# Optimization experiments

Hardware: AMD Instinct MI355X
Metric: run time of the kernel (lower is better)

## Reference

```python
import jax, jax.numpy as jnp
import numpy as np

B, D, LEAVES, MID = 131072, 256, 4, 2


def setup_inputs() -> dict:
    key = jax.random.key(0)
    ks = jax.random.split(key, 5)
    s = 1.0 / np.sqrt(D).astype(np.float32)
    return {
        "x": jax.random.normal(ks[0], (B, D), jnp.float32),
        "Wg": jax.random.normal(ks[1], (D, LEAVES), jnp.float32) * s,
        "bg": jnp.zeros((LEAVES,), jnp.float32),
        "W_leaf": jax.random.normal(ks[2], (LEAVES, D, D), jnp.float32) * s,
        "b_leaf": jnp.zeros((LEAVES, D), jnp.float32),
        "W_mid": jax.random.normal(ks[3], (MID, D, D), jnp.float32) * s,
        "b_mid": jnp.zeros((MID, D), jnp.float32),
        "W_root": jax.random.normal(ks[4], (D, D), jnp.float32) * s,
        "b_root": jnp.zeros((D,), jnp.float32),
    }


def reference(x, Wg, bg, W_leaf, b_leaf, W_mid, b_mid, W_root, b_root):
    # Gate: argmax over leaf experts (torch.max(...).indices over dim=1)
    logits = x @ Wg + bg                      # [B, LEAVES]
    idx = jnp.argmax(logits, axis=1)          # [B] leaf expert per sample
    pidx = idx // 2                           # [B] parent (mid-level) node on the path

    # Leaf level: compute all 4 leaf experts (small E), select routed one.
    h1_all = jax.nn.relu(jnp.einsum('bd,edh->beh', x, W_leaf) + b_leaf)   # [B,4,D]
    h1 = jnp.take_along_axis(h1_all, idx[:, None, None], axis=1)[:, 0]    # [B,D]

    # Mid level: the parent of the selected leaf.
    h2_all = jax.nn.relu(jnp.einsum('bd,pdh->bph', h1, W_mid) + b_mid)    # [B,2,D]
    h2 = jnp.take_along_axis(h2_all, pidx[:, None, None], axis=1)[:, 0]   # [B,D]

    # Root (shared by all paths). end is None -> returned directly.
    return jax.nn.relu(h2 @ W_root + b_root)                              # [B,D]
```

## Files before the change

kernel.cpp:

```cpp
#include <hip/hip_runtime.h>
#include <hip/hip_bf16.h>
#include <stdint.h>

#define B_ROWS 131072
#define DDIM 256
#define GATE_BLOCKS 2048
#define PREPACK_BLOCKS 56
#define TILES_PER_EXPERT 2048

typedef short bf16x8 __attribute__((ext_vector_type(8)));
typedef float f32x4 __attribute__((ext_vector_type(4)));

__device__ __forceinline__ unsigned short f32_to_bf16_rne(float f) {
    union { float f; uint32_t u; } v; v.f = f;
    uint32_t u = v.u;
    u += 0x7fffu + ((u >> 16) & 1u);
    return (unsigned short)(u >> 16);
}

__global__ __launch_bounds__(256) void gate_prepack_kernel(
    const float* __restrict__ x, const float* __restrict__ Wg,
    const float* __restrict__ bg, const float* __restrict__ Wl,
    const float* __restrict__ Wm, const float* __restrict__ Wr,
    int* __restrict__ counts, int* __restrict__ perm,
    unsigned short* __restrict__ wpack)
{
    __shared__ float smemf[4160];
    int t = threadIdx.x;

    if (blockIdx.x >= GATE_BLOCKS) {
        int bid = blockIdx.x - GATE_BLOCKS;
        int m = bid >> 3, s = bid & 7;
        const float* src = (m < 4) ? (Wl + m * 65536)
                         : (m < 6) ? (Wm + (m - 4) * 65536)
                                   : Wr;
        unsigned short* lds = (unsigned short*)smemf;
        #pragma unroll
        for (int i = 0; i < 8; i++) {
            int v = i * 256 + t;
            int kp = v >> 6;
            int n0 = (v & 63) * 4;
            float4 w = *(const float4*)(src + (32 * s + kp) * 256 + n0);
            #pragma unroll
            for (int c = 0; c < 4; c++) {
                int n = n0 + c;
                float val = (c == 0) ? w.x : (c == 1) ? w.y : (c == 2) ? w.z : w.w;
                int o = (n >> 4) * 512 + ((n & 15) + 16 * (kp >> 3)) * 8 + (kp & 7);
                lds[o] = f32_to_bf16_rne(val);
            }
        }
        __syncthreads();
        uint4* outv = (uint4*)(wpack + (m * 8 + s) * 8192);
        const uint4* ldsv = (const uint4*)lds;
        #pragma unroll
        for (int q = 0; q < 4; q++)
            outv[q * 256 + t] = ldsv[q * 256 + t];
        return;
    }

    float* wgl = smemf;
    int* hcount = (int*)(smemf + 1024);
    int* hbase  = (int*)(smemf + 1028);

    ((float4*)wgl)[t] = ((const float4*)Wg)[t];
    if (t < 4) hcount[t] = 0;
    __syncthreads();

    int lrow = t >> 2, sub = t & 3;
    int row = blockIdx.x * 64 + lrow;
    const float* xr = x + (long)row * DDIM;

    double a0 = 0.0, a1 = 0.0, a2 = 0.0, a3 = 0.0;
    #pragma unroll
    for (int i = 0; i < 16; i++) {
        int k0 = i * 16 + sub * 4;
        float4 v = *(const float4*)(xr + k0);
        #pragma unroll
        for (int kk = 0; kk < 4; kk++) {
            float xv = (kk == 0) ? v.x : (kk == 1) ? v.y : (kk == 2) ? v.z : v.w;
            float4 w = *(const float4*)(wgl + (k0 + kk) * 4);
            a0 += (double)xv * (double)w.x;
            a1 += (double)xv * (double)w.y;
            a2 += (double)xv * (double)w.z;
            a3 += (double)xv * (double)w.w;
        }
    }
    a0 += __shfl_xor(a0, 1); a0 += __shfl_xor(a0, 2);
    a1 += __shfl_xor(a1, 1); a1 += __shfl_xor(a1, 2);
    a2 += __shfl_xor(a2, 1); a2 += __shfl_xor(a2, 2);
    a3 += __shfl_xor(a3, 1); a3 += __shfl_xor(a3, 2);

    int myidx = 0, mylpos = 0;
    if (sub == 0) {
        double l0 = a0 + (double)bg[0];
        double l1 = a1 + (double)bg[1];
        double l2 = a2 + (double)bg[2];
        double l3 = a3 + (double)bg[3];
        double best = l0; myidx = 0;
        if (l1 > best) { best = l1; myidx = 1; }
        if (l2 > best) { best = l2; myidx = 2; }
        if (l3 > best) { best = l3; myidx = 3; }
        mylpos = atomicAdd(&hcount[myidx], 1);
    }
    __syncthreads();
    if (t < 4) hbase[t] = atomicAdd(&counts[t], hcount[t]);
    __syncthreads();
    if (sub == 0) perm[myidx * B_ROWS + hbase[myidx] + mylpos] = row;
}

__global__ __launch_bounds__(512, 6) void mlp_kernel(
    const float* __restrict__ x, const unsigned short* __restrict__ wpack,
    const float* __restrict__ b_leaf, const float* __restrict__ b_mid,
    const float* __restrict__ b_root, const int* __restrict__ counts,
    const int* __restrict__ perm, float* __restrict__ out)
{
    __shared__ unsigned short apack[16384];
    __shared__ int rowsLds[64];

    int e = blockIdx.x >> 11;
    int tile = blockIdx.x & 2047;
    int cnt = counts[e];
    int base = tile * 64;
    if (base >= cnt) return;

    int t = threadIdx.x;
    if (t < 64) {
        int src = base + t;
        rowsLds[t] = perm[e * B_ROWS + (src < cnt ? src : base)];
    }
    __syncthreads();

    {
        int r = t >> 3, sub = t & 7;
        const float* xr = x + (long)rowsLds[r] * DDIM;
        int mt = r >> 4, rl = r & 15;
        #pragma unroll
        for (int i = 0; i < 8; i++) {
            int k0 = i * 32 + sub * 4;
            float4 v = *(const float4*)(xr + k0);
            int s = k0 >> 5;
            int fl = rl + 16 * ((k0 >> 3) & 3);
            ushort4 u;
            u.x = f32_to_bf16_rne(v.x);
            u.y = f32_to_bf16_rne(v.y);
            u.z = f32_to_bf16_rne(v.z);
            u.w = f32_to_bf16_rne(v.w);
            *(ushort4*)&apack[((s * 4 + mt) * 64 + fl) * 8 + (k0 & 7)] = u;
        }
    }
    __syncthreads();

    int wv = t >> 6, l = t & 63;
    f32x4 acc[4][2];
    float bias[2];

    auto run_level = [&](const unsigned short* wp, const float* bias_g) {
        #pragma unroll
        for (int nt = 0; nt < 2; nt++)
            bias[nt] = bias_g[(2 * wv + nt) * 16 + (l & 15)];
        f32x4 z = {0.f, 0.f, 0.f, 0.f};
        #pragma unroll
        for (int mt = 0; mt < 4; mt++)
            #pragma unroll
            for (int nt = 0; nt < 2; nt++) acc[mt][nt] = z;

        const bf16x8* wpv = (const bf16x8*)wp;
        #pragma unroll
        for (int s = 0; s < 8; s++) {
            bf16x8 b[2];
            #pragma unroll
            for (int nt = 0; nt < 2; nt++)
                b[nt] = wpv[(s * 16 + 2 * wv + nt) * 64 + l];
            const bf16x8* ap = (const bf16x8*)(apack + s * 4 * 64 * 8);
            #pragma unroll
            for (int mt = 0; mt < 4; mt++) {
                bf16x8 a = ap[mt * 64 + l];
                #pragma unroll
                for (int nt = 0; nt < 2; nt++)
                    acc[mt][nt] = __builtin_amdgcn_mfma_f32_16x16x32_bf16(
                        a, b[nt], acc[mt][nt], 0, 0, 0);
            }
        }
    };

    auto epilogue_lds = [&]() {
        #pragma unroll
        for (int nt = 0; nt < 2; nt++) {
            int col = (2 * wv + nt) * 16 + (l & 15);
            int s = col >> 5;
            int fq = (col >> 3) & 3;
            int j = col & 7;
            #pragma unroll
            for (int mt = 0; mt < 4; mt++) {
                #pragma unroll
                for (int r = 0; r < 4; r++) {
                    float v = fmaxf(acc[mt][nt][r] + bias[nt], 0.f);
                    int fl = ((l >> 4) << 2) + r + 16 * fq;
                    apack[((s * 4 + mt) * 64 + fl) * 8 + j] = f32_to_bf16_rne(v);
                }
            }
        }
    };

    run_level(wpack + e * 65536, b_leaf + e * 256);
    __syncthreads();
    epilogue_lds();
    __syncthreads();

    run_level(wpack + (4 + (e >> 1)) * 65536, b_mid + (e >> 1) * 256);
    __syncthreads();
    epilogue_lds();
    __syncthreads();

    run_level(wpack + 6 * 65536, b_root);
    #pragma unroll
    for (int nt = 0; nt < 2; nt++) {
        int col = (2 * wv + nt) * 16 + (l & 15);
        #pragma unroll
        for (int mt = 0; mt < 4; mt++) {
            #pragma unroll
            for (int r = 0; r < 4; r++) {
                int row_local = mt * 16 + ((l >> 4) << 2) + r;
                if (base + row_local < cnt) {
                    long grow = rowsLds[row_local];
                    out[grow * DDIM + col] = fmaxf(acc[mt][nt][r] + bias[nt], 0.f);
                }
            }
        }
    }
}

extern "C" void kernel_launch(void* const* d_in, const int* in_sizes, int n_in,
                              void* d_out, int out_size, void* d_ws, size_t ws_size,
                              hipStream_t stream) {
    const float* x      = (const float*)d_in[0];
    const float* Wg     = (const float*)d_in[1];
    const float* bg     = (const float*)d_in[2];
    const float* W_leaf = (const float*)d_in[3];
    const float* b_leaf = (const float*)d_in[4];
    const float* W_mid  = (const float*)d_in[5];
    const float* b_mid  = (const float*)d_in[6];
    const float* W_root = (const float*)d_in[7];
    const float* b_root = (const float*)d_in[8];
    float* out = (float*)d_out;

    char* ws = (char*)d_ws;
    int* counts = (int*)ws;
    int* perm = (int*)(ws + 256);
    unsigned short* wpack = (unsigned short*)(ws + (4 << 20));

    hipMemsetAsync(counts, 0, 16, stream);
    gate_prepack_kernel<<<GATE_BLOCKS + PREPACK_BLOCKS, 256, 0, stream>>>(
        x, Wg, bg, W_leaf, W_mid, W_root, counts, perm, wpack);
    mlp_kernel<<<4 * TILES_PER_EXPERT, 512, 0, stream>>>(
        x, wpack, b_leaf, b_mid, b_root, counts, perm, out);
}
```

Measured before the change: 335.1 us.

## Compact MLP grid over expert tiles, use 4-wave blocks, packed bf16 conversion

The grid is now sized to the actual number of 64-row tiles across all four experts, computed from prefix sums of the counts, instead of launching 8192 blocks where most exit early. Blocks drop from 8 waves to 4, so each wave computes 4 N-tiles instead of 2, which doubles the B-fragment loads and accumulator registers per wave. Float-to-bf16 conversion now uses the packed v_cvt_pk_bf16_f32 instruction in both the x staging and the epilogue. The MLP_BLOCKS constant of 2051 is the worst case of the per-expert ceiling sum, and the higher register use may limit occupancy.

```diff
diff --git a/kernel.cpp b/kernel.cpp
--- a/kernel.cpp
+++ b/kernel.cpp
@@ -6,7 +6,7 @@
 #define DDIM 256
 #define GATE_BLOCKS 2048
 #define PREPACK_BLOCKS 56
-#define TILES_PER_EXPERT 2048
+#define MLP_BLOCKS 2051
 
 typedef short bf16x8 __attribute__((ext_vector_type(8)));
 typedef float f32x4 __attribute__((ext_vector_type(4)));
@@ -16,6 +16,12 @@
     uint32_t u = v.u;
     u += 0x7fffu + ((u >> 16) & 1u);
     return (unsigned short)(u >> 16);
+}
+
+__device__ __forceinline__ uint32_t cvt_pk_bf16(float a, float b) {
+    uint32_t r;
+    asm("v_cvt_pk_bf16_f32 %0, %1, %2" : "=v"(r) : "v"(a), "v"(b));
+    return r;
 }
 
 __global__ __launch_bounds__(256) void gate_prepack_kernel(
@@ -108,7 +114,7 @@
     if (sub == 0) perm[myidx * B_ROWS + hbase[myidx] + mylpos] = row;
 }
 
-__global__ __launch_bounds__(512, 6) void mlp_kernel(
+__global__ __launch_bounds__(256, 4) void mlp_kernel(
     const float* __restrict__ x, const unsigned short* __restrict__ wpack,
     const float* __restrict__ b_leaf, const float* __restrict__ b_mid,
     const float* __restrict__ b_root, const int* __restrict__ counts,
@@ -117,11 +123,19 @@
     __shared__ unsigned short apack[16384];
     __shared__ int rowsLds[64];
 
-    int e = blockIdx.x >> 11;
-    int tile = blockIdx.x & 2047;
-    int cnt = counts[e];
+    int c0 = counts[0], c1 = counts[1], c2 = counts[2], c3 = counts[3];
+    int t0 = (c0 + 63) >> 6;
+    int t01 = t0 + ((c1 + 63) >> 6);
+    int t012 = t01 + ((c2 + 63) >> 6);
+    int tall = t012 + ((c3 + 63) >> 6);
+    int bid = blockIdx.x;
+    if (bid >= tall) return;
+    int e, tile, cnt;
+    if (bid < t0)        { e = 0; tile = bid;        cnt = c0; }
+    else if (bid < t01)  { e = 1; tile = bid - t0;   cnt = c1; }
+    else if (bid < t012) { e = 2; tile = bid - t01;  cnt = c2; }
+    else                 { e = 3; tile = bid - t012; cnt = c3; }
     int base = tile * 64;
-    if (base >= cnt) return;
 
     int t = threadIdx.x;
     if (t < 64) {
@@ -131,52 +145,50 @@
     __syncthreads();
 
     {
-        int r = t >> 3, sub = t & 7;
+        int r = t >> 2, sub = t & 3;
         const float* xr = x + (long)rowsLds[r] * DDIM;
         int mt = r >> 4, rl = r & 15;
         #pragma unroll
-        for (int i = 0; i < 8; i++) {
-            int k0 = i * 32 + sub * 4;
+        for (int i = 0; i < 16; i++) {
+            int k0 = i * 16 + sub * 4;
             float4 v = *(const float4*)(xr + k0);
             int s = k0 >> 5;
             int fl = rl + 16 * ((k0 >> 3) & 3);
-            ushort4 u;
-            u.x = f32_to_bf16_rne(v.x);
-            u.y = f32_to_bf16_rne(v.y);
-            u.z = f32_to_bf16_rne(v.z);
-            u.w = f32_to_bf16_rne(v.w);
-            *(ushort4*)&apack[((s * 4 + mt) * 64 + fl) * 8 + (k0 & 7)] = u;
+            uint2 u;
+            u.x = cvt_pk_bf16(v.x, v.y);
+            u.y = cvt_pk_bf16(v.z, v.w);
+            *(uint2*)&apack[((s * 4 + mt) * 64 + fl) * 8 + (k0 & 7)] = u;
         }
     }
     __syncthreads();
 
     int wv = t >> 6, l = t & 63;
-    f32x4 acc[4][2];
-    float bias[2];
+    f32x4 acc[4][4];
+    float bias[4];
 
     auto run_level = [&](const unsigned short* wp, const float* bias_g) {
         #pragma unroll
-        for (int nt = 0; nt < 2; nt++)
-            bias[nt] = bias_g[(2 * wv + nt) * 16 + (l & 15)];
+        for (int nt = 0; nt < 4; nt++)
+            bias[nt] = bias_g[(4 * wv + nt) * 16 + (l & 15)];
         f32x4 z = {0.f, 0.f, 0.f, 0.f};
         #pragma unroll
         for (int mt = 0; mt < 4; mt++)
             #pragma unroll
-            for (int nt = 0; nt < 2; nt++) acc[mt][nt] = z;
+            for (int nt = 0; nt < 4; nt++) acc[mt][nt] = z;
 
         const bf16x8* wpv = (const bf16x8*)wp;
         #pragma unroll
         for (int s = 0; s < 8; s++) {
-            bf16x8 b[2];
-            #pragma unroll
-            for (int nt = 0; nt < 2; nt++)
-                b[nt] = wpv[(s * 16 + 2 * wv + nt) * 64 + l];
+            bf16x8 b[4];
+            #pragma unroll
+            for (int nt = 0; nt < 4; nt++)
+                b[nt] = wpv[(s * 16 + 4 * wv + nt) * 64 + l];
             const bf16x8* ap = (const bf16x8*)(apack + s * 4 * 64 * 8);
             #pragma unroll
             for (int mt = 0; mt < 4; mt++) {
                 bf16x8 a = ap[mt * 64 + l];
                 #pragma unroll
-                for (int nt = 0; nt < 2; nt++)
+                for (int nt = 0; nt < 4; nt++)
                     acc[mt][nt] = __builtin_amdgcn_mfma_f32_16x16x32_bf16(
                         a, b[nt], acc[mt][nt], 0, 0, 0);
             }
@@ -185,19 +197,25 @@
 
     auto epilogue_lds = [&]() {
         #pragma unroll
-        for (int nt = 0; nt < 2; nt++) {
-            int col = (2 * wv + nt) * 16 + (l & 15);
+        for (int nt = 0; nt < 4; nt++) {
+            int col = (4 * wv + nt) * 16 + (l & 15);
             int s = col >> 5;
             int fq = (col >> 3) & 3;
             int j = col & 7;
+            int flb = ((l >> 4) << 2) + 16 * fq;
             #pragma unroll
             for (int mt = 0; mt < 4; mt++) {
-                #pragma unroll
-                for (int r = 0; r < 4; r++) {
-                    float v = fmaxf(acc[mt][nt][r] + bias[nt], 0.f);
-                    int fl = ((l >> 4) << 2) + r + 16 * fq;
-                    apack[((s * 4 + mt) * 64 + fl) * 8 + j] = f32_to_bf16_rne(v);
-                }
+                float v0 = fmaxf(acc[mt][nt][0] + bias[nt], 0.f);
+                float v1 = fmaxf(acc[mt][nt][1] + bias[nt], 0.f);
+                float v2 = fmaxf(acc[mt][nt][2] + bias[nt], 0.f);
+                float v3 = fmaxf(acc[mt][nt][3] + bias[nt], 0.f);
+                uint32_t p01 = cvt_pk_bf16(v0, v1);
+                uint32_t p23 = cvt_pk_bf16(v2, v3);
+                unsigned short* dst = &apack[((s * 4 + mt) * 64 + flb) * 8 + j];
+                dst[0]  = (unsigned short)p01;
+                dst[8]  = (unsigned short)(p01 >> 16);
+                dst[16] = (unsigned short)p23;
+                dst[24] = (unsigned short)(p23 >> 16);
             }
         }
     };
@@ -214,8 +232,8 @@
 
     run_level(wpack + 6 * 65536, b_root);
     #pragma unroll
-    for (int nt = 0; nt < 2; nt++) {
-        int col = (2 * wv + nt) * 16 + (l & 15);
+    for (int nt = 0; nt < 4; nt++) {
+        int col = (4 * wv + nt) * 16 + (l & 15);
         #pragma unroll
         for (int mt = 0; mt < 4; mt++) {
             #pragma unroll
@@ -252,6 +270,6 @@
     hipMemsetAsync(counts, 0, 16, stream);
     gate_prepack_kernel<<<GATE_BLOCKS + PREPACK_BLOCKS, 256, 0, stream>>>(
         x, Wg, bg, W_leaf, W_mid, W_root, counts, perm, wpack);
-    mlp_kernel<<<4 * TILES_PER_EXPERT, 512, 0, stream>>>(
+    mlp_kernel<<<MLP_BLOCKS, 256, 0, stream>>>(
         x, wpack, b_leaf, b_mid, b_root, counts, perm, out);
 }
```

Result: slower. 349.1 us (+4.2%).
